# Optimization experiments

Measured on AMD Instinct MI355X. Metric: run time of the kernel, lower is better.

The kernel has to match this reference:

```python
import jax, jax.numpy as jnp
import numpy as np

B, T, D, K = 16, 8192, 64, 1024


def setup_inputs() -> dict:
    key = jax.random.key(0)
    k1, k2 = jax.random.split(key)
    x = jax.random.normal(k1, (B, T, D, 1), dtype=jnp.float32)
    weight = jax.random.normal(k2, (K, D), dtype=jnp.float32)
    return {"x": x, "weight": weight}


def reference(x, weight):
    # x: [B, T, D, 1] -> squeeze trailing dim -> [B, T, D]
    xs = jnp.squeeze(x, axis=-1)
    x2 = jnp.sum(xs * xs, axis=-1, keepdims=True)          # [B, T, 1]
    e2 = jnp.sum(weight * weight, axis=-1)                 # [K]
    xe = jnp.einsum('btd,kd->btk', xs, weight)             # [B, T, K]
    dist2 = x2 - 2.0 * xe + e2                             # [B, T, K]
    indices = jnp.argmin(dist2, axis=-1)                   # [B, T] int
    quantized = jnp.take(weight, indices, axis=0)          # [B, T, D]
    return quantized, indices
```

## Files before the change

### kernel.cpp

```cpp
#include <hip/hip_runtime.h>

#define MTOK  131072
#define DIMD  64
#define KCODE 1024
#define TPB   128

typedef __bf16 bf16x8 __attribute__((ext_vector_type(8)));
typedef float  f32x4  __attribute__((ext_vector_type(4)));

__device__ __forceinline__ f32x4 mfma16(bf16x8 a, bf16x8 b, f32x4 c) {
    return __builtin_amdgcn_mfma_f32_16x16x32_bf16(a, b, c, 0, 0, 0);
}

__global__ __launch_bounds__(256) void prep_kernel(
    const float* __restrict__ w, __bf16* __restrict__ wpk,
    float* __restrict__ e2n, float* __restrict__ e2) {
    int b   = blockIdx.x;
    int tid = threadIdx.x;
    if (b < 64) {
        int cb  = b;
        int win = tid >> 6, lane = tid & 63;
        int q = lane >> 4, m = lane & 15;
        int k = cb * 16 + m;
        int d0 = (win & 1) * 32 + q * 8;
        const float* src = w + (size_t)k * DIMD + d0;
        float4 v0 = *(const float4*)(src);
        float4 v1 = *(const float4*)(src + 4);
        float f[8] = {v0.x, v0.y, v0.z, v0.w, v1.x, v1.y, v1.z, v1.w};
        bf16x8 o;
#pragma unroll
        for (int j = 0; j < 8; ++j) {
            __bf16 h = (__bf16)f[j];
            o[j] = (win < 2) ? h : (__bf16)(f[j] - (float)h);
        }
        *(bf16x8*)(wpk + ((size_t)(cb * 4 + win) * 64 + lane) * 8) = o;
    } else {
        int k2 = (b - 64) * 256 + tid;
        const float4* row = (const float4*)(w + (size_t)k2 * DIMD);
        float s = 0.f;
#pragma unroll
        for (int i = 0; i < 16; ++i) {
            float4 v = row[i];
            s = fmaf(v.x, v.x, s); s = fmaf(v.y, v.y, s);
            s = fmaf(v.z, v.z, s); s = fmaf(v.w, v.w, s);
        }
        e2[k2]  = s;
        e2n[k2] = -0.5f * s;
    }
}

__global__ __launch_bounds__(256, 4) void vq_main(
    const float* __restrict__ x, const float* __restrict__ wfull,
    const __bf16* __restrict__ wpk, const float* __restrict__ e2n_g,
    const float* __restrict__ e2_g, float* __restrict__ out) {

    const int tid  = threadIdx.x;
    const int blk  = blockIdx.x;
    const int lane = tid & 63;
    const int wv   = tid >> 6;
    const int q    = lane >> 4;
    const int m    = lane & 15;
    const size_t tok0 = (size_t)blk * TPB + wv * 32;

    bf16x8 bx[2][4];
#pragma unroll
    for (int tg = 0; tg < 2; ++tg) {
        const float* xr = x + (tok0 + tg * 16 + m) * DIMD;
#pragma unroll
        for (int h = 0; h < 2; ++h) {
            float4 v0 = *(const float4*)(xr + h * 32 + q * 8);
            float4 v1 = *(const float4*)(xr + h * 32 + q * 8 + 4);
            float f[8] = {v0.x, v0.y, v0.z, v0.w, v1.x, v1.y, v1.z, v1.w};
            bf16x8 hi, lo;
#pragma unroll
            for (int j = 0; j < 8; ++j) {
                __bf16 hh = (__bf16)f[j];
                hi[j] = hh;
                lo[j] = (__bf16)(f[j] - (float)hh);
            }
            bx[tg][h]     = hi;
            bx[tg][2 + h] = lo;
        }
    }

    float b1[2], b2[2]; int i1[2];
#pragma unroll
    for (int tg = 0; tg < 2; ++tg) { b1[tg] = -3e38f; b2[tg] = -3e38f; i1[tg] = 0; }

    const __bf16* wp = wpk + (size_t)lane * 8;
    const float*  ep = e2n_g + q * 4;

    auto compute = [&](const bf16x8& A0, const bf16x8& A1, const bf16x8& A2,
                       const bf16x8& A3, const f32x4& EE, int cbase) {
        __builtin_amdgcn_s_setprio(1);
        f32x4 t0 = mfma16(A0, bx[0][0], EE);
        f32x4 t1 = mfma16(A0, bx[1][0], EE);
        t0 = mfma16(A1, bx[0][1], t0);
        t1 = mfma16(A1, bx[1][1], t1);
        t0 = mfma16(A0, bx[0][2], t0);
        t1 = mfma16(A0, bx[1][2], t1);
        t0 = mfma16(A1, bx[0][3], t0);
        t1 = mfma16(A1, bx[1][3], t1);
        t0 = mfma16(A2, bx[0][0], t0);
        t1 = mfma16(A2, bx[1][0], t1);
        t0 = mfma16(A3, bx[0][1], t0);
        t1 = mfma16(A3, bx[1][1], t1);
        __builtin_amdgcn_s_setprio(0);
#pragma unroll
        for (int r = 0; r < 4; ++r) {
            float a  = t0[r];
            int iv   = cbase + q * 4 + r;
            bool gt  = a > b1[0];
            i1[0] = gt ? iv : i1[0];
            b2[0] = __builtin_amdgcn_fmed3f(a, b1[0], b2[0]);
            b1[0] = fmaxf(a, b1[0]);
        }
#pragma unroll
        for (int r = 0; r < 4; ++r) {
            float a  = t1[r];
            int iv   = cbase + q * 4 + r;
            bool gt  = a > b1[1];
            i1[1] = gt ? iv : i1[1];
            b2[1] = __builtin_amdgcn_fmed3f(a, b1[1], b2[1]);
            b1[1] = fmaxf(a, b1[1]);
        }
    };

    bf16x8 Pa0, Pa1, Pa2, Pa3, Pb0, Pb1, Pb2, Pb3;
    f32x4  Ea, Eb;

    {
        const __bf16* wc = wp;
        Pa0 = *(const bf16x8*)(wc + 0);
        Pa1 = *(const bf16x8*)(wc + 512);
        Pa2 = *(const bf16x8*)(wc + 1024);
        Pa3 = *(const bf16x8*)(wc + 1536);
        Ea  = *(const f32x4*)(ep);
    }

    for (int cb = 0; cb < 64; cb += 2) {
        {
            const __bf16* wc = wp + (size_t)(cb + 1) * 2048;
            Pb0 = *(const bf16x8*)(wc + 0);
            Pb1 = *(const bf16x8*)(wc + 512);
            Pb2 = *(const bf16x8*)(wc + 1024);
            Pb3 = *(const bf16x8*)(wc + 1536);
            Eb  = *(const f32x4*)(ep + (cb + 1) * 16);
        }
        compute(Pa0, Pa1, Pa2, Pa3, Ea, cb * 16);
        if (cb + 2 < 64) {
            const __bf16* wc = wp + (size_t)(cb + 2) * 2048;
            Pa0 = *(const bf16x8*)(wc + 0);
            Pa1 = *(const bf16x8*)(wc + 512);
            Pa2 = *(const bf16x8*)(wc + 1024);
            Pa3 = *(const bf16x8*)(wc + 1536);
            Ea  = *(const f32x4*)(ep + (cb + 2) * 16);
        }
        compute(Pb0, Pb1, Pb2, Pb3, Eb, (cb + 1) * 16);
    }

    float B1f[2], B2f[2]; int I1f[2];
#pragma unroll
    for (int tg = 0; tg < 2; ++tg) {
        float B1 = b1[tg], B2 = b2[tg]; int I1 = i1[tg];
#pragma unroll
        for (int mask = 16; mask <= 32; mask <<= 1) {
            float ob1 = __shfl_xor(B1, mask);
            float ob2 = __shfl_xor(B2, mask);
            int   oi  = __shfl_xor(I1, mask);
            bool take = (ob1 > B1) || (ob1 == B1 && oi < I1);
            B2 = fmaxf(fminf(ob1, B1), fmaxf(ob2, B2));
            I1 = take ? oi : I1;
            B1 = fmaxf(ob1, B1);
        }
        B1f[tg] = B1; B2f[tg] = B2; I1f[tg] = I1;
    }

    int myidx;
    {
        int src = lane & 15;
        int v0 = __shfl(I1f[0], src);
        int v1 = __shfl(I1f[1], src);
        myidx = ((lane >> 4) & 1) ? v1 : v0;
    }

#pragma unroll
    for (int tg = 0; tg < 2; ++tg) {
        unsigned long long msk =
            __ballot((lane < 16) && (B1f[tg] - B2f[tg] < 2e-3f));
        while (msk) {
            int mm = __ffsll((unsigned long long)msk) - 1;
            msk &= msk - 1;
            int tloc = tg * 16 + mm;
            const float4* xr = (const float4*)(x + (tok0 + tloc) * DIMD);
            float bv = 3e38f; int bi = 0;
            for (int j = 0; j < 16; ++j) {
                int k = lane * 16 + j;
                const float4* wr = (const float4*)(wfull + (size_t)k * DIMD);
                float s = 0.f;
#pragma unroll
                for (int i = 0; i < 16; ++i) {
                    float4 xv = xr[i], wv4 = wr[i];
                    s = fmaf(xv.x, wv4.x, s); s = fmaf(xv.y, wv4.y, s);
                    s = fmaf(xv.z, wv4.z, s); s = fmaf(xv.w, wv4.w, s);
                }
                float dv = fmaf(-2.f, s, e2_g[k]);
                if (dv < bv) { bv = dv; bi = k; }
            }
#pragma unroll
            for (int mask2 = 1; mask2 <= 32; mask2 <<= 1) {
                float ov = __shfl_xor(bv, mask2);
                int   oi = __shfl_xor(bi, mask2);
                bool take = (ov < bv) || (ov == bv && oi < bi);
                bv = take ? ov : bv;
                bi = take ? oi : bi;
            }
            myidx = (lane == tloc) ? bi : myidx;
        }
    }

    if (lane < 32)
        __builtin_nontemporal_store((float)myidx,
                                    out + (size_t)MTOK * DIMD + tok0 + lane);

    {
        float* obase = out + tok0 * DIMD;
#pragma unroll
        for (int j = 0; j < 8; ++j) {
            int srcl = j * 4 + (lane >> 4);
            int gi   = __shfl(myidx, srcl);
            f32x4 v = *(const f32x4*)(wfull + (size_t)gi * DIMD + (lane & 15) * 4);
            __builtin_nontemporal_store(v, (f32x4*)(obase + j * 256 + lane * 4));
        }
    }
}

extern "C" void kernel_launch(void* const* d_in, const int* in_sizes, int n_in,
                              void* d_out, int out_size, void* d_ws, size_t ws_size,
                              hipStream_t stream) {
    const float* x = (const float*)d_in[0];
    const float* w = (const float*)d_in[1];
    float* out = (float*)d_out;

    __bf16* wpk = (__bf16*)d_ws;
    float*  e2n = (float*)((char*)d_ws + 262144);
    float*  e2  = (float*)((char*)d_ws + 266240);

    prep_kernel<<<68, 256, 0, stream>>>(w, wpk, e2n, e2);
    vq_main<<<MTOK / TPB, 256, 0, stream>>>(x, w, wpk, e2n, e2, out);
}
```

Before: 153.0 us.

## Process 64 tokens per wave to reuse codebook fragments across four token groups

Each wave now handles four 16-token groups instead of two, so every codebook fragment loaded from global memory feeds twice as many MFMAs. Block token count doubles and the grid halves, while the argmin, fallback and gather/store epilogue are widened to four groups. The goal is to cut codebook load traffic and loop overhead per token. In exchange, register pressure rises, occupancy drops (launch bound 4 to 2 blocks per CU), and there are fewer blocks to spread across CUs.

```diff
diff --git a/kernel.cpp b/kernel.cpp
--- a/kernel.cpp
+++ b/kernel.cpp
@@ -3,7 +3,7 @@
 #define MTOK  131072
 #define DIMD  64
 #define KCODE 1024
-#define TPB   128
+#define TPB   256
 
 typedef __bf16 bf16x8 __attribute__((ext_vector_type(8)));
 typedef float  f32x4  __attribute__((ext_vector_type(4)));
@@ -49,7 +49,7 @@
     }
 }
 
-__global__ __launch_bounds__(256, 4) void vq_main(
+__global__ __launch_bounds__(256, 2) void vq_main(
     const float* __restrict__ x, const float* __restrict__ wfull,
     const __bf16* __restrict__ wpk, const float* __restrict__ e2n_g,
     const float* __restrict__ e2_g, float* __restrict__ out) {
@@ -60,11 +60,11 @@
     const int wv   = tid >> 6;
     const int q    = lane >> 4;
     const int m    = lane & 15;
-    const size_t tok0 = (size_t)blk * TPB + wv * 32;
-
-    bf16x8 bx[2][4];
-#pragma unroll
-    for (int tg = 0; tg < 2; ++tg) {
+    const size_t tok0 = (size_t)blk * TPB + wv * 64;
+
+    bf16x8 bx[4][4];
+#pragma unroll
+    for (int tg = 0; tg < 4; ++tg) {
         const float* xr = x + (tok0 + tg * 16 + m) * DIMD;
 #pragma unroll
         for (int h = 0; h < 2; ++h) {
@@ -83,9 +83,9 @@
         }
     }
 
-    float b1[2], b2[2]; int i1[2];
-#pragma unroll
-    for (int tg = 0; tg < 2; ++tg) { b1[tg] = -3e38f; b2[tg] = -3e38f; i1[tg] = 0; }
+    float b1[4], b2[4]; int i1[4];
+#pragma unroll
+    for (int tg = 0; tg < 4; ++tg) { b1[tg] = -3e38f; b2[tg] = -3e38f; i1[tg] = 0; }
 
     const __bf16* wp = wpk + (size_t)lane * 8;
     const float*  ep = e2n_g + q * 4;
@@ -95,34 +95,41 @@
         __builtin_amdgcn_s_setprio(1);
         f32x4 t0 = mfma16(A0, bx[0][0], EE);
         f32x4 t1 = mfma16(A0, bx[1][0], EE);
+        f32x4 t2 = mfma16(A0, bx[2][0], EE);
+        f32x4 t3 = mfma16(A0, bx[3][0], EE);
         t0 = mfma16(A1, bx[0][1], t0);
         t1 = mfma16(A1, bx[1][1], t1);
+        t2 = mfma16(A1, bx[2][1], t2);
+        t3 = mfma16(A1, bx[3][1], t3);
         t0 = mfma16(A0, bx[0][2], t0);
         t1 = mfma16(A0, bx[1][2], t1);
+        t2 = mfma16(A0, bx[2][2], t2);
+        t3 = mfma16(A0, bx[3][2], t3);
         t0 = mfma16(A1, bx[0][3], t0);
         t1 = mfma16(A1, bx[1][3], t1);
+        t2 = mfma16(A1, bx[2][3], t2);
+        t3 = mfma16(A1, bx[3][3], t3);
         t0 = mfma16(A2, bx[0][0], t0);
         t1 = mfma16(A2, bx[1][0], t1);
+        t2 = mfma16(A2, bx[2][0], t2);
+        t3 = mfma16(A2, bx[3][0], t3);
         t0 = mfma16(A3, bx[0][1], t0);
         t1 = mfma16(A3, bx[1][1], t1);
+        t2 = mfma16(A3, bx[2][1], t2);
+        t3 = mfma16(A3, bx[3][1], t3);
         __builtin_amdgcn_s_setprio(0);
-#pragma unroll
-        for (int r = 0; r < 4; ++r) {
-            float a  = t0[r];
-            int iv   = cbase + q * 4 + r;
-            bool gt  = a > b1[0];
-            i1[0] = gt ? iv : i1[0];
-            b2[0] = __builtin_amdgcn_fmed3f(a, b1[0], b2[0]);
-            b1[0] = fmaxf(a, b1[0]);
-        }
-#pragma unroll
-        for (int r = 0; r < 4; ++r) {
-            float a  = t1[r];
-            int iv   = cbase + q * 4 + r;
-            bool gt  = a > b1[1];
-            i1[1] = gt ? iv : i1[1];
-            b2[1] = __builtin_amdgcn_fmed3f(a, b1[1], b2[1]);
-            b1[1] = fmaxf(a, b1[1]);
+        f32x4 tt[4] = {t0, t1, t2, t3};
+#pragma unroll
+        for (int tg = 0; tg < 4; ++tg) {
+#pragma unroll
+            for (int r = 0; r < 4; ++r) {
+                float a  = tt[tg][r];
+                int iv   = cbase + q * 4 + r;
+                bool gt  = a > b1[tg];
+                i1[tg] = gt ? iv : i1[tg];
+                b2[tg] = __builtin_amdgcn_fmed3f(a, b1[tg], b2[tg]);
+                b1[tg] = fmaxf(a, b1[tg]);
+            }
         }
     };
 
@@ -159,9 +166,9 @@
         compute(Pb0, Pb1, Pb2, Pb3, Eb, (cb + 1) * 16);
     }
 
-    float B1f[2], B2f[2]; int I1f[2];
-#pragma unroll
-    for (int tg = 0; tg < 2; ++tg) {
+    float B1f[4], B2f[4]; int I1f[4];
+#pragma unroll
+    for (int tg = 0; tg < 4; ++tg) {
         float B1 = b1[tg], B2 = b2[tg]; int I1 = i1[tg];
 #pragma unroll
         for (int mask = 16; mask <= 32; mask <<= 1) {
@@ -181,11 +188,16 @@
         int src = lane & 15;
         int v0 = __shfl(I1f[0], src);
         int v1 = __shfl(I1f[1], src);
-        myidx = ((lane >> 4) & 1) ? v1 : v0;
-    }
-
-#pragma unroll
-    for (int tg = 0; tg < 2; ++tg) {
+        int v2 = __shfl(I1f[2], src);
+        int v3 = __shfl(I1f[3], src);
+        int hi2 = lane >> 4;
+        int va = (hi2 & 1) ? v1 : v0;
+        int vb = (hi2 & 1) ? v3 : v2;
+        myidx = (hi2 & 2) ? vb : va;
+    }
+
+#pragma unroll
+    for (int tg = 0; tg < 4; ++tg) {
         unsigned long long msk =
             __ballot((lane < 16) && (B1f[tg] - B2f[tg] < 2e-3f));
         while (msk) {
@@ -219,14 +231,13 @@
         }
     }
 
-    if (lane < 32)
-        __builtin_nontemporal_store((float)myidx,
-                                    out + (size_t)MTOK * DIMD + tok0 + lane);
+    __builtin_nontemporal_store((float)myidx,
+                                out + (size_t)MTOK * DIMD + tok0 + lane);
 
     {
         float* obase = out + tok0 * DIMD;
 #pragma unroll
-        for (int j = 0; j < 8; ++j) {
+        for (int j = 0; j < 16; ++j) {
             int srcl = j * 4 + (lane >> 4);
             int gi   = __shfl(myidx, srcl);
             f32x4 v = *(const f32x4*)(wfull + (size_t)gi * DIMD + (lane & 15) * 4);
```

After: 142.9 us. 1.07x faster.

## Switch distance GEMM to 32x32x16 MFMA with repacked codebook layout

Applied to the files above, without the earlier changes.

Replaces the 16x16x32 bf16 MFMA tiles (two 16-token groups per wave) with a single 32x32x16 MFMA tile covering all 32 tokens of a wave and 32 codes per step, repacking the codebook in the prep kernel to match. The split-bf16 products are accumulated into two independent accumulators to shorten the dependent MFMA chain, and the argmin reduction simplifies to a single cross-half shuffle. The aim is less per-code operand traffic and fewer reduction instructions. The cost is larger 16-wide accumulators, which raises register pressure, plus a changed prefetch pattern with only a single weight buffer.

```diff
diff --git a/kernel.cpp b/kernel.cpp
--- a/kernel.cpp
+++ b/kernel.cpp
@@ -7,9 +7,10 @@
 
 typedef __bf16 bf16x8 __attribute__((ext_vector_type(8)));
 typedef float  f32x4  __attribute__((ext_vector_type(4)));
-
-__device__ __forceinline__ f32x4 mfma16(bf16x8 a, bf16x8 b, f32x4 c) {
-    return __builtin_amdgcn_mfma_f32_16x16x32_bf16(a, b, c, 0, 0, 0);
+typedef float  f32x16 __attribute__((ext_vector_type(16)));
+
+__device__ __forceinline__ f32x16 mfma32(bf16x8 a, bf16x8 b, f32x16 c) {
+    return __builtin_amdgcn_mfma_f32_32x32x16_bf16(a, b, c, 0, 0, 0);
 }
 
 __global__ __launch_bounds__(256) void prep_kernel(
@@ -18,12 +19,13 @@
     int b   = blockIdx.x;
     int tid = threadIdx.x;
     if (b < 64) {
-        int cb  = b;
-        int win = tid >> 6, lane = tid & 63;
-        int q = lane >> 4, m = lane & 15;
-        int k = cb * 16 + m;
-        int d0 = (win & 1) * 32 + q * 8;
-        const float* src = w + (size_t)k * DIMD + d0;
+        int cb32 = b >> 1, half = b & 1;
+        int idx  = half * 4 + (tid >> 6);
+        int term = idx >> 2, ks = idx & 3;
+        int lane = tid & 63;
+        int code = cb32 * 32 + (lane & 31);
+        int k0   = ks * 16 + (lane >> 5) * 8;
+        const float* src = w + (size_t)code * DIMD + k0;
         float4 v0 = *(const float4*)(src);
         float4 v1 = *(const float4*)(src + 4);
         float f[8] = {v0.x, v0.y, v0.z, v0.w, v1.x, v1.y, v1.z, v1.w};
@@ -31,9 +33,9 @@
 #pragma unroll
         for (int j = 0; j < 8; ++j) {
             __bf16 h = (__bf16)f[j];
-            o[j] = (win < 2) ? h : (__bf16)(f[j] - (float)h);
-        }
-        *(bf16x8*)(wpk + ((size_t)(cb * 4 + win) * 64 + lane) * 8) = o;
+            o[j] = (term == 0) ? h : (__bf16)(f[j] - (float)h);
+        }
+        *(bf16x8*)(wpk + (size_t)cb32 * 4096 + term * 2048 + ks * 512 + lane * 8) = o;
     } else {
         int k2 = (b - 64) * 256 + tid;
         const float4* row = (const float4*)(w + (size_t)k2 * DIMD);
@@ -58,140 +60,103 @@
     const int blk  = blockIdx.x;
     const int lane = tid & 63;
     const int wv   = tid >> 6;
-    const int q    = lane >> 4;
-    const int m    = lane & 15;
+    const int col  = lane & 31;
+    const int hi   = lane >> 5;
     const size_t tok0 = (size_t)blk * TPB + wv * 32;
 
-    bf16x8 bx[2][4];
-#pragma unroll
-    for (int tg = 0; tg < 2; ++tg) {
-        const float* xr = x + (tok0 + tg * 16 + m) * DIMD;
-#pragma unroll
-        for (int h = 0; h < 2; ++h) {
-            float4 v0 = *(const float4*)(xr + h * 32 + q * 8);
-            float4 v1 = *(const float4*)(xr + h * 32 + q * 8 + 4);
+    bf16x8 XH[4], XL[4];
+    {
+        const float* xr = x + (tok0 + col) * DIMD;
+#pragma unroll
+        for (int ks = 0; ks < 4; ++ks) {
+            float4 v0 = *(const float4*)(xr + ks * 16 + hi * 8);
+            float4 v1 = *(const float4*)(xr + ks * 16 + hi * 8 + 4);
             float f[8] = {v0.x, v0.y, v0.z, v0.w, v1.x, v1.y, v1.z, v1.w};
-            bf16x8 hi, lo;
+            bf16x8 h8, l8;
 #pragma unroll
             for (int j = 0; j < 8; ++j) {
                 __bf16 hh = (__bf16)f[j];
-                hi[j] = hh;
-                lo[j] = (__bf16)(f[j] - (float)hh);
-            }
-            bx[tg][h]     = hi;
-            bx[tg][2 + h] = lo;
-        }
-    }
-
-    float b1[2], b2[2]; int i1[2];
-#pragma unroll
-    for (int tg = 0; tg < 2; ++tg) { b1[tg] = -3e38f; b2[tg] = -3e38f; i1[tg] = 0; }
-
-    const __bf16* wp = wpk + (size_t)lane * 8;
-    const float*  ep = e2n_g + q * 4;
-
-    auto compute = [&](const bf16x8& A0, const bf16x8& A1, const bf16x8& A2,
-                       const bf16x8& A3, const f32x4& EE, int cbase) {
+                h8[j] = hh;
+                l8[j] = (__bf16)(f[j] - (float)hh);
+            }
+            XH[ks] = h8;
+            XL[ks] = l8;
+        }
+    }
+
+    float b1 = -3e38f, b2 = -3e38f; int i1 = 0;
+
+    const __bf16* wpl = wpk + (size_t)lane * 8;
+
+    bf16x8 WH[4], WL[4];
+#pragma unroll
+    for (int ks = 0; ks < 4; ++ks) {
+        WH[ks] = *(const bf16x8*)(wpl + ks * 512);
+        WL[ks] = *(const bf16x8*)(wpl + 2048 + ks * 512);
+    }
+
+    for (int cb32 = 0; cb32 < 32; ++cb32) {
+        union { f32x16 v; f32x4 q[4]; } EE;
+#pragma unroll
+        for (int g = 0; g < 4; ++g)
+            EE.q[g] = *(const f32x4*)(e2n_g + cb32 * 32 + hi * 4 + g * 8);
+
+        f32x16 acc  = EE.v;
+        f32x16 acc2 = {};
         __builtin_amdgcn_s_setprio(1);
-        f32x4 t0 = mfma16(A0, bx[0][0], EE);
-        f32x4 t1 = mfma16(A0, bx[1][0], EE);
-        t0 = mfma16(A1, bx[0][1], t0);
-        t1 = mfma16(A1, bx[1][1], t1);
-        t0 = mfma16(A0, bx[0][2], t0);
-        t1 = mfma16(A0, bx[1][2], t1);
-        t0 = mfma16(A1, bx[0][3], t0);
-        t1 = mfma16(A1, bx[1][3], t1);
-        t0 = mfma16(A2, bx[0][0], t0);
-        t1 = mfma16(A2, bx[1][0], t1);
-        t0 = mfma16(A3, bx[0][1], t0);
-        t1 = mfma16(A3, bx[1][1], t1);
+        acc  = mfma32(WH[0], XH[0], acc);
+        acc2 = mfma32(WL[0], XH[0], acc2);
+        acc  = mfma32(WH[1], XH[1], acc);
+        acc2 = mfma32(WL[1], XH[1], acc2);
+        acc  = mfma32(WH[2], XH[2], acc);
+        acc2 = mfma32(WL[2], XH[2], acc2);
+        acc  = mfma32(WH[3], XH[3], acc);
+        acc2 = mfma32(WL[3], XH[3], acc2);
+        acc  = mfma32(WH[0], XL[0], acc);
+        acc  = mfma32(WH[1], XL[1], acc);
+        acc  = mfma32(WH[2], XL[2], acc);
+        acc  = mfma32(WH[3], XL[3], acc);
         __builtin_amdgcn_s_setprio(0);
-#pragma unroll
-        for (int r = 0; r < 4; ++r) {
-            float a  = t0[r];
-            int iv   = cbase + q * 4 + r;
-            bool gt  = a > b1[0];
-            i1[0] = gt ? iv : i1[0];
-            b2[0] = __builtin_amdgcn_fmed3f(a, b1[0], b2[0]);
-            b1[0] = fmaxf(a, b1[0]);
-        }
-#pragma unroll
-        for (int r = 0; r < 4; ++r) {
-            float a  = t1[r];
-            int iv   = cbase + q * 4 + r;
-            bool gt  = a > b1[1];
-            i1[1] = gt ? iv : i1[1];
-            b2[1] = __builtin_amdgcn_fmed3f(a, b1[1], b2[1]);
-            b1[1] = fmaxf(a, b1[1]);
-        }
-    };
-
-    bf16x8 Pa0, Pa1, Pa2, Pa3, Pb0, Pb1, Pb2, Pb3;
-    f32x4  Ea, Eb;
-
-    {
-        const __bf16* wc = wp;
-        Pa0 = *(const bf16x8*)(wc + 0);
-        Pa1 = *(const bf16x8*)(wc + 512);
-        Pa2 = *(const bf16x8*)(wc + 1024);
-        Pa3 = *(const bf16x8*)(wc + 1536);
-        Ea  = *(const f32x4*)(ep);
-    }
-
-    for (int cb = 0; cb < 64; cb += 2) {
-        {
-            const __bf16* wc = wp + (size_t)(cb + 1) * 2048;
-            Pb0 = *(const bf16x8*)(wc + 0);
-            Pb1 = *(const bf16x8*)(wc + 512);
-            Pb2 = *(const bf16x8*)(wc + 1024);
-            Pb3 = *(const bf16x8*)(wc + 1536);
-            Eb  = *(const f32x4*)(ep + (cb + 1) * 16);
-        }
-        compute(Pa0, Pa1, Pa2, Pa3, Ea, cb * 16);
-        if (cb + 2 < 64) {
-            const __bf16* wc = wp + (size_t)(cb + 2) * 2048;
-            Pa0 = *(const bf16x8*)(wc + 0);
-            Pa1 = *(const bf16x8*)(wc + 512);
-            Pa2 = *(const bf16x8*)(wc + 1024);
-            Pa3 = *(const bf16x8*)(wc + 1536);
-            Ea  = *(const f32x4*)(ep + (cb + 2) * 16);
-        }
-        compute(Pb0, Pb1, Pb2, Pb3, Eb, (cb + 1) * 16);
-    }
-
-    float B1f[2], B2f[2]; int I1f[2];
-#pragma unroll
-    for (int tg = 0; tg < 2; ++tg) {
-        float B1 = b1[tg], B2 = b2[tg]; int I1 = i1[tg];
-#pragma unroll
-        for (int mask = 16; mask <= 32; mask <<= 1) {
-            float ob1 = __shfl_xor(B1, mask);
-            float ob2 = __shfl_xor(B2, mask);
-            int   oi  = __shfl_xor(I1, mask);
-            bool take = (ob1 > B1) || (ob1 == B1 && oi < I1);
-            B2 = fmaxf(fminf(ob1, B1), fmaxf(ob2, B2));
-            I1 = take ? oi : I1;
-            B1 = fmaxf(ob1, B1);
-        }
-        B1f[tg] = B1; B2f[tg] = B2; I1f[tg] = I1;
-    }
-
-    int myidx;
-    {
-        int src = lane & 15;
-        int v0 = __shfl(I1f[0], src);
-        int v1 = __shfl(I1f[1], src);
-        myidx = ((lane >> 4) & 1) ? v1 : v0;
-    }
-
-#pragma unroll
-    for (int tg = 0; tg < 2; ++tg) {
+
+        if (cb32 + 1 < 32) {
+            const __bf16* wn = wpl + (size_t)(cb32 + 1) * 4096;
+#pragma unroll
+            for (int ks = 0; ks < 4; ++ks) {
+                WL[ks] = *(const bf16x8*)(wn + 2048 + ks * 512);
+                WH[ks] = *(const bf16x8*)(wn + ks * 512);
+            }
+        }
+
+#pragma unroll
+        for (int r = 0; r < 16; ++r) {
+            const int rowoff = (r & 3) + 8 * (r >> 2);
+            float a  = acc[r] + acc2[r];
+            int iv   = cb32 * 32 + hi * 4 + rowoff;
+            bool gt  = a > b1;
+            i1 = gt ? iv : i1;
+            b2 = __builtin_amdgcn_fmed3f(a, b1, b2);
+            b1 = fmaxf(a, b1);
+        }
+    }
+
+    {
+        float ob1 = __shfl_xor(b1, 32);
+        float ob2 = __shfl_xor(b2, 32);
+        int   oi  = __shfl_xor(i1, 32);
+        bool take = (ob1 > b1) || (ob1 == b1 && oi < i1);
+        b2 = fmaxf(fminf(ob1, b1), fmaxf(ob2, b2));
+        i1 = take ? oi : i1;
+        b1 = fmaxf(ob1, b1);
+    }
+    int myidx = i1;
+
+    {
         unsigned long long msk =
-            __ballot((lane < 16) && (B1f[tg] - B2f[tg] < 2e-3f));
+            __ballot((lane < 32) && (b1 - b2 < 2e-3f));
         while (msk) {
             int mm = __ffsll((unsigned long long)msk) - 1;
             msk &= msk - 1;
-            int tloc = tg * 16 + mm;
+            int tloc = mm;
             const float4* xr = (const float4*)(x + (tok0 + tloc) * DIMD);
             float bv = 3e38f; int bi = 0;
             for (int j = 0; j < 16; ++j) {
```

New measurement: 167.9 us. 9.7% more time.

## Stage packed codebook in LDS with 1024-thread blocks and software-pipelined MFMA

Applied to the files above, without the earlier changes.

Blocks grow to 1024 threads (512 tokens), and the packed bf16 codebook is staged into LDS in two 128KB halves using global_load_lds, instead of each wave streaming it from global/L2. The loop is restructured so the argmin tracking for one chunk overlaps the MFMA chains of the next chunk. This aims to cut repeated L2 traffic and load latency for the codebook. In exchange it adds barriers, a mid-kernel reload, and about 132KB of LDS per block, which limits occupancy to one block per CU.

```diff
diff --git a/kernel.cpp b/kernel.cpp
--- a/kernel.cpp
+++ b/kernel.cpp
@@ -3,13 +3,19 @@
 #define MTOK  131072
 #define DIMD  64
 #define KCODE 1024
-#define TPB   128
+#define TPB   512
 
 typedef __bf16 bf16x8 __attribute__((ext_vector_type(8)));
 typedef float  f32x4  __attribute__((ext_vector_type(4)));
 
 __device__ __forceinline__ f32x4 mfma16(bf16x8 a, bf16x8 b, f32x4 c) {
     return __builtin_amdgcn_mfma_f32_16x16x32_bf16(a, b, c, 0, 0, 0);
+}
+
+__device__ __forceinline__ void g2l16(const void* g, void* l) {
+    __builtin_amdgcn_global_load_lds(
+        (const __attribute__((address_space(1))) unsigned int*)g,
+        (__attribute__((address_space(3))) unsigned int*)l, 16, 0, 0);
 }
 
 __global__ __launch_bounds__(256) void prep_kernel(
@@ -49,10 +55,13 @@
     }
 }
 
-__global__ __launch_bounds__(256, 4) void vq_main(
+__global__ __launch_bounds__(1024, 4) void vq_main(
     const float* __restrict__ x, const float* __restrict__ wfull,
     const __bf16* __restrict__ wpk, const float* __restrict__ e2n_g,
     const float* __restrict__ e2_g, float* __restrict__ out) {
+
+    __shared__ __align__(16) __bf16 ldsW[65536];
+    __shared__ __align__(16) float  ldsE[KCODE];
 
     const int tid  = threadIdx.x;
     const int blk  = blockIdx.x;
@@ -62,6 +71,16 @@
     const int m    = lane & 15;
     const size_t tok0 = (size_t)blk * TPB + wv * 32;
 
+    {
+        const char* gw = (const char*)wpk;
+        char* lw = (char*)ldsW;
+#pragma unroll
+        for (int j = 0; j < 8; ++j)
+            g2l16(gw + j * 16384 + tid * 16, lw + j * 16384 + tid * 16);
+        if (tid < 256)
+            g2l16((const char*)e2n_g + tid * 16, (char*)ldsE + tid * 16);
+    }
+
     bf16x8 bx[2][4];
 #pragma unroll
     for (int tg = 0; tg < 2; ++tg) {
@@ -87,14 +106,11 @@
 #pragma unroll
     for (int tg = 0; tg < 2; ++tg) { b1[tg] = -3e38f; b2[tg] = -3e38f; i1[tg] = 0; }
 
-    const __bf16* wp = wpk + (size_t)lane * 8;
-    const float*  ep = e2n_g + q * 4;
-
-    auto compute = [&](const bf16x8& A0, const bf16x8& A1, const bf16x8& A2,
-                       const bf16x8& A3, const f32x4& EE, int cbase) {
+    auto chains = [&](const bf16x8& A0, const bf16x8& A1, const bf16x8& A2,
+                      const bf16x8& A3, const f32x4& EE, f32x4& t0, f32x4& t1) {
         __builtin_amdgcn_s_setprio(1);
-        f32x4 t0 = mfma16(A0, bx[0][0], EE);
-        f32x4 t1 = mfma16(A0, bx[1][0], EE);
+        t0 = mfma16(A0, bx[0][0], EE);
+        t1 = mfma16(A0, bx[1][0], EE);
         t0 = mfma16(A1, bx[0][1], t0);
         t1 = mfma16(A1, bx[1][1], t1);
         t0 = mfma16(A0, bx[0][2], t0);
@@ -106,6 +122,9 @@
         t0 = mfma16(A3, bx[0][1], t0);
         t1 = mfma16(A3, bx[1][1], t1);
         __builtin_amdgcn_s_setprio(0);
+    };
+
+    auto tracker = [&](const f32x4& t0, const f32x4& t1, int cbase) {
 #pragma unroll
         for (int r = 0; r < 4; ++r) {
             float a  = t0[r];
@@ -126,37 +145,66 @@
         }
     };
 
-    bf16x8 Pa0, Pa1, Pa2, Pa3, Pb0, Pb1, Pb2, Pb3;
-    f32x4  Ea, Eb;
-
-    {
-        const __bf16* wc = wp;
-        Pa0 = *(const bf16x8*)(wc + 0);
-        Pa1 = *(const bf16x8*)(wc + 512);
-        Pa2 = *(const bf16x8*)(wc + 1024);
-        Pa3 = *(const bf16x8*)(wc + 1536);
-        Ea  = *(const f32x4*)(ep);
-    }
-
-    for (int cb = 0; cb < 64; cb += 2) {
+    __syncthreads();
+
+    for (int pass = 0; pass < 2; ++pass) {
+        if (pass) {
+            __syncthreads();
+            const char* gw = (const char*)wpk + 131072;
+            char* lw = (char*)ldsW;
+#pragma unroll
+            for (int j = 0; j < 8; ++j)
+                g2l16(gw + j * 16384 + tid * 16, lw + j * 16384 + tid * 16);
+            __syncthreads();
+        }
+
+        const __bf16* wb = ldsW + lane * 8;
+        const int eb  = pass * 512 + q * 4;
+        const int cb0 = pass * 32;
+
+        bf16x8 Wa0, Wa1, Wa2, Wa3, Wb0, Wb1, Wb2, Wb3;
+        f32x4  Ea, Eb, tA0, tA1, tB0, tB1;
+
+        Wa0 = *(const bf16x8*)(wb + 0);
+        Wa1 = *(const bf16x8*)(wb + 512);
+        Wa2 = *(const bf16x8*)(wb + 1024);
+        Wa3 = *(const bf16x8*)(wb + 1536);
+        Ea  = *(const f32x4*)&ldsE[eb];
+        chains(Wa0, Wa1, Wa2, Wa3, Ea, tA0, tA1);
+
+        for (int cb = 1; cb <= 29; cb += 2) {
+            {
+                const __bf16* wc = wb + cb * 2048;
+                Wb0 = *(const bf16x8*)(wc + 0);
+                Wb1 = *(const bf16x8*)(wc + 512);
+                Wb2 = *(const bf16x8*)(wc + 1024);
+                Wb3 = *(const bf16x8*)(wc + 1536);
+                Eb  = *(const f32x4*)&ldsE[eb + cb * 16];
+                tracker(tA0, tA1, (cb0 + cb - 1) * 16);
+                chains(Wb0, Wb1, Wb2, Wb3, Eb, tB0, tB1);
+            }
+            {
+                const __bf16* wc = wb + (cb + 1) * 2048;
+                Wa0 = *(const bf16x8*)(wc + 0);
+                Wa1 = *(const bf16x8*)(wc + 512);
+                Wa2 = *(const bf16x8*)(wc + 1024);
+                Wa3 = *(const bf16x8*)(wc + 1536);
+                Ea  = *(const f32x4*)&ldsE[eb + (cb + 1) * 16];
+                tracker(tB0, tB1, (cb0 + cb) * 16);
+                chains(Wa0, Wa1, Wa2, Wa3, Ea, tA0, tA1);
+            }
+        }
         {
-            const __bf16* wc = wp + (size_t)(cb + 1) * 2048;
-            Pb0 = *(const bf16x8*)(wc + 0);
-            Pb1 = *(const bf16x8*)(wc + 512);
-            Pb2 = *(const bf16x8*)(wc + 1024);
-            Pb3 = *(const bf16x8*)(wc + 1536);
-            Eb  = *(const f32x4*)(ep + (cb + 1) * 16);
-        }
-        compute(Pa0, Pa1, Pa2, Pa3, Ea, cb * 16);
-        if (cb + 2 < 64) {
-            const __bf16* wc = wp + (size_t)(cb + 2) * 2048;
-            Pa0 = *(const bf16x8*)(wc + 0);
-            Pa1 = *(const bf16x8*)(wc + 512);
-            Pa2 = *(const bf16x8*)(wc + 1024);
-            Pa3 = *(const bf16x8*)(wc + 1536);
-            Ea  = *(const f32x4*)(ep + (cb + 2) * 16);
-        }
-        compute(Pb0, Pb1, Pb2, Pb3, Eb, (cb + 1) * 16);
+            const __bf16* wc = wb + 31 * 2048;
+            Wb0 = *(const bf16x8*)(wc + 0);
+            Wb1 = *(const bf16x8*)(wc + 512);
+            Wb2 = *(const bf16x8*)(wc + 1024);
+            Wb3 = *(const bf16x8*)(wc + 1536);
+            Eb  = *(const f32x4*)&ldsE[eb + 31 * 16];
+            tracker(tA0, tA1, (cb0 + 30) * 16);
+            chains(Wb0, Wb1, Wb2, Wb3, Eb, tB0, tB1);
+            tracker(tB0, tB1, (cb0 + 31) * 16);
+        }
     }
 
     float B1f[2], B2f[2]; int I1f[2];
@@ -247,5 +295,5 @@
     float*  e2  = (float*)((char*)d_ws + 266240);
 
     prep_kernel<<<68, 256, 0, stream>>>(w, wpk, e2n, e2);
-    vq_main<<<MTOK / TPB, 256, 0, stream>>>(x, w, wpk, e2n, e2, out);
-}
+    vq_main<<<MTOK / TPB, 1024, 0, stream>>>(x, w, wpk, e2n, e2, out);
+}
```

Result: no change. 152.1 us (-0.6%).
